# Performance work log

Measured on AMD Instinct MI355X. Metric: run time of the kernel, lower is better.

The kernel has to match this reference:

```python
import jax, jax.numpy as jnp
import numpy as np

ROPE_BASE = 1000000.0
EPS = 1e-6
N_HEADS = 8


def apply_rope(x, base=ROPE_BASE):
    # x: [b, s, h, d]
    b, s, h, d = x.shape
    half = d // 2
    theta = 1.0 / base ** (2 * jnp.arange(half) / d)          # [half]
    angles = jnp.arange(s)[:, None] * theta[None, :]          # [s, half]
    cos = jnp.cos(angles)[None, :, None, :]                   # [1, s, 1, half]
    sin = jnp.sin(angles)[None, :, None, :]
    x1, x2 = jnp.split(x, 2, axis=-1)
    return jnp.concatenate([x1 * cos - x2 * sin, x1 * sin + x2 * cos], axis=-1)


def setup_inputs() -> dict:
    key = jax.random.key(0)
    ks = jax.random.split(key, 5)
    b, s, dim = 2, 4096, 512
    x = jax.random.normal(ks[0], (b, s, dim), dtype=jnp.float32)
    scale = jnp.ones((dim,), dtype=jnp.float32)
    init = 1.0 / np.sqrt(dim)
    Wq = jax.random.normal(ks[1], (dim, dim), dtype=jnp.float32) * init
    Wk = jax.random.normal(ks[2], (dim, dim), dtype=jnp.float32) * init
    Wv = jax.random.normal(ks[3], (dim, dim), dtype=jnp.float32) * init
    Wo = jax.random.normal(ks[4], (dim, dim), dtype=jnp.float32) * init
    return {"x": x, "scale": scale, "Wq": Wq, "Wk": Wk, "Wv": Wv, "Wo": Wo}


def reference(x, scale, Wq, Wk, Wv, Wo):
    b, s, dim = x.shape
    h = N_HEADS
    dh = dim // h
    # RMSNorm (use_fast_variance=False path)
    variance = jnp.mean(x ** 2, axis=-1, keepdims=True)
    x_norm = x / jnp.sqrt(variance + EPS) * scale
    # Projections (flax Linear: y = x @ kernel, kernel [in, out])
    q = (x_norm @ Wq).reshape(b, s, h, dh)
    k = (x_norm @ Wk).reshape(b, s, h, dh)
    v = (x_norm @ Wv).reshape(b, s, h, dh)
    q = apply_rope(q)
    k = apply_rope(k)
    scores = jnp.einsum('bthd,bshd->bhts', q, k) / jnp.sqrt(jnp.float32(dh))
    mask = jnp.triu(jnp.full((s, s), -jnp.inf, dtype=jnp.float32), k=1)
    scores = scores + mask[None, None, :, :]
    attn = jax.nn.softmax(scores, axis=-1)
    out = jnp.einsum('bhts,bshd->bthd', attn, v).reshape(b, s, dim)
    return out @ Wo
```

## Files before the change

### kernel.cpp

```cpp
#include <hip/hip_runtime.h>
#include <hip/hip_bf16.h>

typedef _Float16 f16;
typedef _Float16 f16x2 __attribute__((ext_vector_type(2)));
typedef _Float16 f16x4 __attribute__((ext_vector_type(4)));
typedef _Float16 f16x8 __attribute__((ext_vector_type(8)));
typedef float f32x4 __attribute__((ext_vector_type(4)));

#define S_LEN 4096
#define DIM   512
#define NH    8
#define DH    64
#define BATCH 2
#define BHDIM (BATCH*NH)

#define QSCALE 0.18033688011112042f

__device__ __forceinline__ void gld16(const f16* g, f16* l) {
#if __has_builtin(__builtin_amdgcn_global_load_lds)
  __builtin_amdgcn_global_load_lds((const __attribute__((address_space(1))) void*)g,
                                   (__attribute__((address_space(3))) void*)l, 16, 0, 0);
#else
  *(f16x8*)l = *(const f16x8*)g;
#endif
}

__device__ __forceinline__ float fexp2(float x) {
#if __has_builtin(__builtin_amdgcn_exp2f)
  return __builtin_amdgcn_exp2f(x);
#else
  return exp2f(x);
#endif
}

__device__ __forceinline__ f16x2 pk2(float a, float b) {
#if __has_builtin(__builtin_amdgcn_cvt_pkrtz)
  auto r = __builtin_amdgcn_cvt_pkrtz(a, b);
  f16x2 o; __builtin_memcpy(&o, &r, sizeof(o));
  return o;
#else
  f16x2 r; r[0] = (f16)a; r[1] = (f16)b; return r;
#endif
}

__global__ __launch_bounds__(256) void rmsnorm_kernel(
    const float* __restrict__ x, const float* __restrict__ scale,
    f16* __restrict__ xn) {
  int row = blockIdx.x;
  int tid = threadIdx.x;
  const float* xr = x + (size_t)row * DIM;
  float2 v = *(const float2*)(xr + tid*2);
  float ss = v.x*v.x + v.y*v.y;
  #pragma unroll
  for (int off = 32; off > 0; off >>= 1) ss += __shfl_down(ss, off);
  __shared__ float red[4];
  if ((tid & 63) == 0) red[tid >> 6] = ss;
  __syncthreads();
  float tot = red[0] + red[1] + red[2] + red[3];
  float inv = rsqrtf(tot * (1.0f/DIM) + 1e-6f);
  float2 s = *(const float2*)(scale + tid*2);
  xn[(size_t)row*DIM + tid*2+0] = (f16)(v.x*inv*s.x);
  xn[(size_t)row*DIM + tid*2+1] = (f16)(v.y*inv*s.y);
}

__global__ void transpose_kernel(const float* __restrict__ Wq,
                                 const float* __restrict__ Wk,
                                 const float* __restrict__ Wv,
                                 const float* __restrict__ Wo,
                                 f16* __restrict__ wt_qkv, f16* __restrict__ wo_t) {
  __shared__ f16 tile[32][33];
  int mat = blockIdx.z;
  const float* src = (mat == 0) ? Wq : (mat == 1) ? Wk : (mat == 2) ? Wv : Wo;
  f16* dst = (mat < 3) ? (wt_qkv + (size_t)mat*DIM*DIM) : wo_t;
  int k0 = blockIdx.y * 32, n0 = blockIdx.x * 32;
  int tx = threadIdx.x, ty = threadIdx.y;
  #pragma unroll
  for (int i = 0; i < 32; i += 8)
    tile[ty+i][tx] = (f16)src[(size_t)(k0+ty+i)*DIM + n0+tx];
  __syncthreads();
  #pragma unroll
  for (int i = 0; i < 32; i += 8)
    dst[(size_t)(n0+ty+i)*DIM + k0+tx] = tile[tx][ty+i];
}

__global__ __launch_bounds__(256) void rope_table_kernel(float* __restrict__ ctab,
                                                         float* __restrict__ stab) {
  int idx = blockIdx.x*256 + threadIdx.x;
  int t = idx >> 5, d = idx & 31;
  float theta = exp2f(-(float)d * (19.931568569324174f / 32.0f));
  float sv, cv;
  sincosf((float)t * theta, &sv, &cv);
  ctab[idx] = cv; stab[idx] = sv;
}

__device__ __forceinline__ void gemm128_acc(
    const f16* __restrict__ A, const f16* __restrict__ Bt,
    int m0, int n0, f16* As, f16* Bs, f32x4 (&acc)[4][4]) {
  const int tid = threadIdx.x;
  const int wave = tid >> 6, lane = tid & 63;
  const int l16 = lane & 15, quad = lane >> 4;
  const int mrow = (wave & 1) * 64, ncol = (wave >> 1) * 64;
  const int srow = tid >> 3;
  const int gc = (tid & 7) ^ ((tid >> 3) & 7);

  for (int k0 = 0; k0 < DIM; k0 += 64) {
    if (k0) __syncthreads();
    #pragma unroll
    for (int i = 0; i < 4; i++) {
      gld16(A  + (size_t)(m0 + i*32 + srow)*DIM + k0 + gc*8, As + i*2048 + tid*8);
      gld16(Bt + (size_t)(n0 + i*32 + srow)*DIM + k0 + gc*8, Bs + i*2048 + tid*8);
    }
    __syncthreads();
    #pragma unroll
    for (int kc = 0; kc < 2; kc++) {
      f16x8 a[4], b[4];
      #pragma unroll
      for (int mt = 0; mt < 4; mt++) {
        int row = mrow + mt*16 + l16;
        a[mt] = *(const f16x8*)(As + row*64 + (((quad + 4*kc) ^ (l16 & 7)) * 8));
      }
      #pragma unroll
      for (int nt = 0; nt < 4; nt++) {
        int row = ncol + nt*16 + l16;
        b[nt] = *(const f16x8*)(Bs + row*64 + (((quad + 4*kc) ^ (l16 & 7)) * 8));
      }
      #pragma unroll
      for (int mt = 0; mt < 4; mt++)
        #pragma unroll
        for (int nt = 0; nt < 4; nt++)
          acc[mt][nt] = __builtin_amdgcn_mfma_f32_16x16x32_f16(a[mt], b[nt], acc[mt][nt], 0, 0, 0);
    }
  }
}

__global__ __launch_bounds__(256) void qkv_gemm_kernel(
    const f16* __restrict__ xn, const f16* __restrict__ wt,
    const float* __restrict__ ctab, const float* __restrict__ stab,
    f16* __restrict__ qbuf, f16* __restrict__ kbuf, f16* __restrict__ vt) {
  __shared__ __align__(16) f16 As[128*64], Bs[128*64];
  int m0 = blockIdx.x * 128, n0 = blockIdx.y * 128;
  f32x4 acc[4][4] = {};
  gemm128_acc(xn, wt, m0, n0, As, Bs, acc);

  const int tid = threadIdx.x;
  const int wave = tid >> 6, lane = tid & 63;
  const int l16 = lane & 15, quad = lane >> 4;
  int ncol = n0 + (wave >> 1) * 64;
  int which = ncol >> 9;
  int head = (ncol >> 6) & 7;
  int mbase = m0 + (wave & 1) * 64;

  if (which <= 1) {
    #pragma unroll
    for (int mt = 0; mt < 4; mt++)
      #pragma unroll
      for (int nt = 0; nt < 2; nt++) {
        int d = nt*16 + l16;
        #pragma unroll
        for (int r = 0; r < 4; r++) {
          int t = (mbase + mt*16 + quad*4 + r) & 4095;
          float cv = ctab[t*32 + d], sv = stab[t*32 + d];
          float x1 = acc[mt][nt][r], x2 = acc[mt][nt+2][r];
          acc[mt][nt][r]   = x1*cv - x2*sv;
          acc[mt][nt+2][r] = x1*sv + x2*cv;
        }
      }
  }
  if (which < 2) {
    float osc = (which == 0) ? QSCALE : 1.0f;
    f16* dst = which ? kbuf : qbuf;
    #pragma unroll
    for (int mt = 0; mt < 4; mt++)
      #pragma unroll
      for (int nt = 0; nt < 4; nt++)
        #pragma unroll
        for (int r = 0; r < 4; r++) {
          int m = mbase + mt*16 + quad*4 + r;
          int b = m >> 12, t = m & 4095;
          dst[(((size_t)(b*NH + head))*S_LEN + t)*DH + nt*16 + l16] = (f16)(acc[mt][nt][r]*osc);
        }
  } else {
    #pragma unroll
    for (int mt = 0; mt < 4; mt++)
      #pragma unroll
      for (int nt = 0; nt < 4; nt++) {
        int m = mbase + mt*16 + quad*4;
        int b = m >> 12, t = m & 4095;
        int d = nt*16 + l16;
        f16x4 v4 = {(f16)acc[mt][nt][0], (f16)acc[mt][nt][1],
                    (f16)acc[mt][nt][2], (f16)acc[mt][nt][3]};
        *(f16x4*)(vt + ((size_t)((b*NH + head)*DH + d))*S_LEN + t) = v4;
      }
  }
}

__global__ __launch_bounds__(128, 2) void attn_kernel(
    const f16* __restrict__ qbuf, const f16* __restrict__ kbuf,
    const f16* __restrict__ vtb, f16* __restrict__ ao) {
  int bid = blockIdx.x;
  int bh  = bid & 15;
  int p   = bid >> 4;

  int tid = threadIdx.x;
  int wave = tid >> 6, lane = tid & 63;
  int l16 = lane & 15, quad = lane >> 4;

  const f16* Q = qbuf + (size_t)bh*S_LEN*DH;
  const f16* K = kbuf + (size_t)bh*S_LEN*DH;
  const f16* V = vtb  + (size_t)bh*DH*S_LEN;

  int bandv[2] = {127 - p, p};
  int tcnt[2]  = {((127 - p) >> 1) + 1, (p >> 1) + 1};
  int rbase[2] = {bandv[0]*32 + wave*16, bandv[1]*32 + wave*16};

  f16x8 qa[2][2];
  #pragma unroll
  for (int bi = 0; bi < 2; bi++) {
    const f16* qrow = Q + (size_t)(rbase[bi] + l16)*DH + quad*8;
    qa[bi][0] = *(const f16x8*)(qrow);
    qa[bi][1] = *(const f16x8*)(qrow + 32);
  }

  f32x4 o[2][4] = {};
  float m_i[2] = {-1e30f, -1e30f};
  float l_i[2] = {0.f, 0.f};

  __shared__ __align__(16) f16 kt[2*4096];
  __shared__ __align__(16) f16 vs[2*4096];

  const int gcs = (tid & 7) ^ ((tid >> 3) & 7);
  const int srow = tid >> 3;

  #define STAGE(buf, kv)                                                        \
    do {                                                                        \
      f16* ktb = kt + (buf)*4096;                                               \
      f16* vsb = vs + (buf)*4096;                                               \
      _Pragma("unroll")                                                         \
      for (int n = 0; n < 4; n++) {                                             \
        gld16(K + (size_t)((kv) + n*16 + srow)*DH + gcs*8, ktb + n*1024 + tid*8);\
        gld16(V + (size_t)(n*16 + srow)*S_LEN + (kv) + gcs*8, vsb + n*1024 + tid*8);\
      }                                                                         \
    } while (0)

  STAGE(0, 0);
  __syncthreads();

  int nth = tcnt[0];
  for (int it = 0; it < nth; ++it) {
    int kv0 = it * 64;
    int cur = it & 1;
    if (it + 1 < nth) STAGE(cur ^ 1, kv0 + 64);

    const f16* ktc = kt + cur*4096;
    const f16* vsc = vs + cur*4096;

    bool act1 = (it < tcnt[1]);
    bool dia0 = (it == tcnt[0] - 1), dia1 = (it == tcnt[1] - 1);
    int ntl0 = dia0 ? ((bandv[0] & 1) ? 4 : 2) : 4;
    int ntl1 = act1 ? (dia1 ? ((bandv[1] & 1) ? 4 : 2) : 4) : 0;

    f32x4 st[2][4];
    #pragma unroll
    for (int nt = 0; nt < 4; nt++) {
      bool n0 = (nt < ntl0), n1 = (nt < ntl1);
      if (n0 || n1) {
        int row = nt*16 + l16;
        f16x8 kf0 = *(const f16x8*)(ktc + row*64 + (((quad)     ^ (row & 7))*8));
        f16x8 kf1 = *(const f16x8*)(ktc + row*64 + (((quad + 4) ^ (row & 7))*8));
        if (n0) {
          f32x4 z = {};
          z = __builtin_amdgcn_mfma_f32_16x16x32_f16(kf0, qa[0][0], z, 0, 0, 0);
          st[0][nt] = __builtin_amdgcn_mfma_f32_16x16x32_f16(kf1, qa[0][1], z, 0, 0, 0);
        }
        if (n1) {
          f32x4 z = {};
          z = __builtin_amdgcn_mfma_f32_16x16x32_f16(kf0, qa[1][0], z, 0, 0, 0);
          st[1][nt] = __builtin_amdgcn_mfma_f32_16x16x32_f16(kf1, qa[1][1], z, 0, 0, 0);
        }
      }
    }

    f16x8 pa[2][2];
    #pragma unroll
    for (int bi = 0; bi < 2; bi++) {
      int ntl = bi ? ntl1 : ntl0;
      if (ntl == 0) continue;
      bool diag = bi ? dia1 : dia0;
      int qglob = rbase[bi] + l16;
      float rmx = -1e30f;
      #pragma unroll
      for (int nt = 0; nt < 4; nt++) {
        if (nt >= ntl) continue;
        if (diag) {
          int kb = kv0 + nt*16 + quad*4;
          #pragma unroll
          for (int r = 0; r < 4; r++) {
            float v = st[bi][nt][r];
            if (kb + r > qglob) v = -1e30f;
            st[bi][nt][r] = v;
            rmx = fmaxf(rmx, v);
          }
        } else {
          #pragma unroll
          for (int r = 0; r < 4; r++) rmx = fmaxf(rmx, st[bi][nt][r]);
        }
      }
      rmx = fmaxf(rmx, __shfl_xor(rmx, 16));
      rmx = fmaxf(rmx, __shfl_xor(rmx, 32));
      if (!__all(rmx <= m_i[bi] + 8.0f)) {
        float mnew = fmaxf(m_i[bi], rmx);
        float alpha = fexp2(m_i[bi] - mnew);
        m_i[bi] = mnew;
        float al[4];
        #pragma unroll
        for (int r = 0; r < 4; r++) al[r] = __shfl(alpha, quad*4 + r);
        #pragma unroll
        for (int dnt = 0; dnt < 4; dnt++)
          #pragma unroll
          for (int r = 0; r < 4; r++) o[bi][dnt][r] *= al[r];
        l_i[bi] *= alpha;
      }
      float mref = m_i[bi];
      int kcl = ntl >> 1;
      float rs = 0.f;
      #pragma unroll
      for (int c = 0; c < 2; c++) {
        if (c >= kcl) continue;
        float e0 = fexp2(st[bi][2*c  ][0] - mref);
        float e1 = fexp2(st[bi][2*c  ][1] - mref);
        float e2 = fexp2(st[bi][2*c  ][2] - mref);
        float e3 = fexp2(st[bi][2*c  ][3] - mref);
        float e4 = fexp2(st[bi][2*c+1][0] - mref);
        float e5 = fexp2(st[bi][2*c+1][1] - mref);
        float e6 = fexp2(st[bi][2*c+1][2] - mref);
        float e7 = fexp2(st[bi][2*c+1][3] - mref);
        rs += ((e0+e1)+(e2+e3)) + ((e4+e5)+(e6+e7));
        f16x4 h0 = __builtin_shufflevector(pk2(e0,e1), pk2(e2,e3), 0,1,2,3);
        f16x4 h1 = __builtin_shufflevector(pk2(e4,e5), pk2(e6,e7), 0,1,2,3);
        pa[bi][c] = __builtin_shufflevector(h0, h1, 0,1,2,3,4,5,6,7);
      }
      l_i[bi] += rs;
    }

    int kcl0 = ntl0 >> 1, kcl1 = ntl1 >> 1;
    #pragma unroll
    for (int c = 0; c < 2; c++) {
      bool lv0 = (c < kcl0), lv1 = (c < kcl1);
      if (!lv0 && !lv1) continue;
      #pragma unroll
      for (int dnt = 0; dnt < 4; dnt++) {
        int vr = dnt*16 + l16;
        int iLo = vr*64 + (((c*4 +     (quad>>1)) ^ (vr & 7))*8) + (quad & 1)*4;
        int iHi = vr*64 + (((c*4 + 2 + (quad>>1)) ^ (vr & 7))*8) + (quad & 1)*4;
        f16x4 lo = *(const f16x4*)(vsc + iLo);
        f16x4 hi = *(const f16x4*)(vsc + iHi);
        f16x8 vf = __builtin_shufflevector(lo, hi, 0,1,2,3,4,5,6,7);
        if (lv0) o[0][dnt] = __builtin_amdgcn_mfma_f32_16x16x32_f16(pa[0][c], vf, o[0][dnt], 0, 0, 0);
        if (lv1) o[1][dnt] = __builtin_amdgcn_mfma_f32_16x16x32_f16(pa[1][c], vf, o[1][dnt], 0, 0, 0);
      }
    }

    __syncthreads();
  }
  #undef STAGE

  int b = bh >> 3, h = bh & 7;
  #pragma unroll
  for (int bi = 0; bi < 2; bi++) {
    float lf = l_i[bi];
    lf += __shfl_xor(lf, 16);
    lf += __shfl_xor(lf, 32);
    float lr[4];
    #pragma unroll
    for (int r = 0; r < 4; r++) lr[r] = __shfl(lf, quad*4 + r);
    #pragma unroll
    for (int r = 0; r < 4; r++) {
      float invl = 1.0f / lr[r];
      int t = rbase[bi] + quad*4 + r;
      size_t rowoff = ((size_t)(b*S_LEN + t))*DIM + h*DH;
      #pragma unroll
      for (int dnt = 0; dnt < 4; dnt++)
        ao[rowoff + dnt*16 + l16] = (f16)(o[bi][dnt][r]*invl);
    }
  }
}

__global__ __launch_bounds__(256) void out_gemm_kernel(
    const f16* __restrict__ ao, const f16* __restrict__ wot,
    float* __restrict__ out) {
  __shared__ __align__(16) f16 As[128*64], Bs[128*64];
  int m0 = blockIdx.x * 128, n0 = blockIdx.y * 128;
  f32x4 acc[4][4] = {};
  gemm128_acc(ao, wot, m0, n0, As, Bs, acc);

  const int tid = threadIdx.x;
  const int wave = tid >> 6, lane = tid & 63;
  const int l16 = lane & 15, quad = lane >> 4;
  int ncol = n0 + (wave >> 1) * 64;
  int mbase = m0 + (wave & 1) * 64;
  #pragma unroll
  for (int mt = 0; mt < 4; mt++)
    #pragma unroll
    for (int nt = 0; nt < 4; nt++)
      #pragma unroll
      for (int r = 0; r < 4; r++)
        out[(size_t)(mbase + mt*16 + quad*4 + r)*DIM + ncol + nt*16 + l16] = acc[mt][nt][r];
}

extern "C" void kernel_launch(void* const* d_in, const int* in_sizes, int n_in,
                              void* d_out, int out_size, void* d_ws, size_t ws_size,
                              hipStream_t stream) {
  const float* x     = (const float*)d_in[0];
  const float* scale = (const float*)d_in[1];
  const float* Wq    = (const float*)d_in[2];
  const float* Wk    = (const float*)d_in[3];
  const float* Wv    = (const float*)d_in[4];
  const float* Wo    = (const float*)d_in[5];
  float* out = (float*)d_out;

  const size_t ROWS = (size_t)BATCH * S_LEN;
  char* ws = (char*)d_ws;
  f16* xn     = (f16*)ws;  ws += ROWS * DIM * sizeof(f16);
  f16* wt_qkv = (f16*)ws;  ws += (size_t)3 * DIM * DIM * sizeof(f16);
  f16* wo_t   = (f16*)ws;  ws += (size_t)DIM * DIM * sizeof(f16);
  f16* qb     = (f16*)ws;  ws += (size_t)BHDIM * S_LEN * DH * sizeof(f16);
  f16* kb     = (f16*)ws;  ws += (size_t)BHDIM * S_LEN * DH * sizeof(f16);
  f16* vt     = (f16*)ws;  ws += (size_t)BHDIM * S_LEN * DH * sizeof(f16);
  float* ctab = (float*)ws; ws += (size_t)S_LEN * 32 * sizeof(float);
  float* stab = (float*)ws; ws += (size_t)S_LEN * 32 * sizeof(float);
  f16* ao     = xn;

  size_t need = (size_t)(ws - (char*)d_ws);
  if (ws_size < need) return;

  rmsnorm_kernel   <<<ROWS, 256, 0, stream>>>(x, scale, xn);
  transpose_kernel <<<dim3(16,16,4), dim3(32,8), 0, stream>>>(Wq, Wk, Wv, Wo, wt_qkv, wo_t);
  rope_table_kernel<<<512, 256, 0, stream>>>(ctab, stab);
  qkv_gemm_kernel  <<<dim3(64,12), 256, 0, stream>>>(xn, wt_qkv, ctab, stab, qb, kb, vt);
  attn_kernel      <<<1024, 128, 0, stream>>>(qb, kb, vt, ao);
  out_gemm_kernel  <<<dim3(64,4), 256, 0, stream>>>(ao, wo_t, out);
}
```

Measured before the change: 205.5 us.

## Split attention KV range across two blocks and merge partials in new kernel

Doubles the attention grid: each block now handles either the even or the odd 64-key tiles for its query bands, and writes partial outputs plus row max and row sum. A new merge kernel combines the two halves with log-sum-exp weights before the output GEMM. V is now stored in a pre-permuted layout so each lane loads its V fragments straight from global memory, which drops the V LDS staging. The row-max shuffles are also deferred to the rescale branch. This aims to raise occupancy and parallelism, at the cost of an extra kernel launch, f16 partial round-trips through memory, and uncached global V loads.

```diff
diff --git a/kernel.cpp b/kernel.cpp
--- a/kernel.cpp
+++ b/kernel.cpp
@@ -13,6 +13,7 @@
 #define DH    64
 #define BATCH 2
 #define BHDIM (BATCH*NH)
+#define ROWS2 (BHDIM*S_LEN)
 
 #define QSCALE 0.18033688011112042f
 
@@ -185,21 +186,26 @@
       #pragma unroll
       for (int nt = 0; nt < 4; nt++) {
         int m = mbase + mt*16 + quad*4;
-        int b = m >> 12, t = m & 4095;
+        int b = m >> 12, tcol = m & 4095;
+        int grp = tcol & ~63;
+        int pos = ((mt >> 1)*4 + quad)*8 + (mt & 1)*4;
         int d = nt*16 + l16;
         f16x4 v4 = {(f16)acc[mt][nt][0], (f16)acc[mt][nt][1],
                     (f16)acc[mt][nt][2], (f16)acc[mt][nt][3]};
-        *(f16x4*)(vt + ((size_t)((b*NH + head)*DH + d))*S_LEN + t) = v4;
+        *(f16x4*)(vt + ((size_t)((b*NH + head)*DH + d))*S_LEN + grp + pos) = v4;
       }
   }
 }
 
 __global__ __launch_bounds__(128, 2) void attn_kernel(
     const f16* __restrict__ qbuf, const f16* __restrict__ kbuf,
-    const f16* __restrict__ vtb, f16* __restrict__ ao) {
+    const f16* __restrict__ vtb, f16* __restrict__ po,
+    float* __restrict__ pm, float* __restrict__ pl) {
   int bid = blockIdx.x;
   int bh  = bid & 15;
-  int p   = bid >> 4;
+  int pp  = bid >> 4;
+  int p   = pp >> 1;
+  int hf  = pp & 1;
 
   int tid = threadIdx.x;
   int wave = tid >> 6, lane = tid & 63;
@@ -210,8 +216,10 @@
   const f16* V = vtb  + (size_t)bh*DH*S_LEN;
 
   int bandv[2] = {127 - p, p};
-  int tcnt[2]  = {((127 - p) >> 1) + 1, (p >> 1) + 1};
+  int T0 = ((127 - p) >> 1) + 1, T1 = (p >> 1) + 1;
   int rbase[2] = {bandv[0]*32 + wave*16, bandv[1]*32 + wave*16};
+
+  int nloc = (T0 - hf + 1) >> 1;
 
   f16x8 qa[2][2];
   #pragma unroll
@@ -226,36 +234,37 @@
   float l_i[2] = {0.f, 0.f};
 
   __shared__ __align__(16) f16 kt[2*4096];
-  __shared__ __align__(16) f16 vs[2*4096];
 
   const int gcs = (tid & 7) ^ ((tid >> 3) & 7);
   const int srow = tid >> 3;
 
-  #define STAGE(buf, kv)                                                        \
+  #define STAGEK(buf, kv)                                                       \
     do {                                                                        \
       f16* ktb = kt + (buf)*4096;                                               \
-      f16* vsb = vs + (buf)*4096;                                               \
       _Pragma("unroll")                                                         \
-      for (int n = 0; n < 4; n++) {                                             \
+      for (int n = 0; n < 4; n++)                                               \
         gld16(K + (size_t)((kv) + n*16 + srow)*DH + gcs*8, ktb + n*1024 + tid*8);\
-        gld16(V + (size_t)(n*16 + srow)*S_LEN + (kv) + gcs*8, vsb + n*1024 + tid*8);\
-      }                                                                         \
     } while (0)
 
-  STAGE(0, 0);
+  STAGEK(0, hf*64);
   __syncthreads();
 
-  int nth = tcnt[0];
-  for (int it = 0; it < nth; ++it) {
-    int kv0 = it * 64;
-    int cur = it & 1;
-    if (it + 1 < nth) STAGE(cur ^ 1, kv0 + 64);
+  for (int itl = 0; itl < nloc; ++itl) {
+    int g = 2*itl + hf;
+    int kv0 = g*64;
+    int cur = itl & 1;
+    if (itl + 1 < nloc) STAGEK(cur ^ 1, kv0 + 128);
+
+    f16x8 pv[2][4];
+    #pragma unroll
+    for (int c = 0; c < 2; c++)
+      #pragma unroll
+      for (int dnt = 0; dnt < 4; dnt++)
+        pv[c][dnt] = *(const f16x8*)(V + (size_t)(dnt*16 + l16)*S_LEN + kv0 + (c*4 + quad)*8);
 
     const f16* ktc = kt + cur*4096;
-    const f16* vsc = vs + cur*4096;
-
-    bool act1 = (it < tcnt[1]);
-    bool dia0 = (it == tcnt[0] - 1), dia1 = (it == tcnt[1] - 1);
+    bool act1 = (g < T1);
+    bool dia0 = (g == T0 - 1), dia1 = (g == T1 - 1);
     int ntl0 = dia0 ? ((bandv[0] & 1) ? 4 : 2) : 4;
     int ntl1 = act1 ? (dia1 ? ((bandv[1] & 1) ? 4 : 2) : 4) : 0;
 
@@ -305,10 +314,10 @@
           for (int r = 0; r < 4; r++) rmx = fmaxf(rmx, st[bi][nt][r]);
         }
       }
-      rmx = fmaxf(rmx, __shfl_xor(rmx, 16));
-      rmx = fmaxf(rmx, __shfl_xor(rmx, 32));
       if (!__all(rmx <= m_i[bi] + 8.0f)) {
-        float mnew = fmaxf(m_i[bi], rmx);
+        float rfull = fmaxf(rmx, __shfl_xor(rmx, 16));
+        rfull = fmaxf(rfull, __shfl_xor(rfull, 32));
+        float mnew = fmaxf(m_i[bi], rfull);
         float alpha = fexp2(m_i[bi] - mnew);
         m_i[bi] = mnew;
         float al[4];
@@ -349,40 +358,68 @@
       if (!lv0 && !lv1) continue;
       #pragma unroll
       for (int dnt = 0; dnt < 4; dnt++) {
-        int vr = dnt*16 + l16;
-        int iLo = vr*64 + (((c*4 +     (quad>>1)) ^ (vr & 7))*8) + (quad & 1)*4;
-        int iHi = vr*64 + (((c*4 + 2 + (quad>>1)) ^ (vr & 7))*8) + (quad & 1)*4;
-        f16x4 lo = *(const f16x4*)(vsc + iLo);
-        f16x4 hi = *(const f16x4*)(vsc + iHi);
-        f16x8 vf = __builtin_shufflevector(lo, hi, 0,1,2,3,4,5,6,7);
-        if (lv0) o[0][dnt] = __builtin_amdgcn_mfma_f32_16x16x32_f16(pa[0][c], vf, o[0][dnt], 0, 0, 0);
-        if (lv1) o[1][dnt] = __builtin_amdgcn_mfma_f32_16x16x32_f16(pa[1][c], vf, o[1][dnt], 0, 0, 0);
+        if (lv0) o[0][dnt] = __builtin_amdgcn_mfma_f32_16x16x32_f16(pa[0][c], pv[c][dnt], o[0][dnt], 0, 0, 0);
+        if (lv1) o[1][dnt] = __builtin_amdgcn_mfma_f32_16x16x32_f16(pa[1][c], pv[c][dnt], o[1][dnt], 0, 0, 0);
       }
     }
 
     __syncthreads();
   }
-  #undef STAGE
-
-  int b = bh >> 3, h = bh & 7;
+  #undef STAGEK
+
   #pragma unroll
   for (int bi = 0; bi < 2; bi++) {
     float lf = l_i[bi];
     lf += __shfl_xor(lf, 16);
     lf += __shfl_xor(lf, 32);
-    float lr[4];
+    if (quad == 0) {
+      int t = rbase[bi] + l16;
+      pm[(size_t)(hf*BHDIM + bh)*S_LEN + t] = m_i[bi];
+      pl[(size_t)(hf*BHDIM + bh)*S_LEN + t] = lf;
+    }
+    float lr[4], mrow[4];
     #pragma unroll
     for (int r = 0; r < 4; r++) lr[r] = __shfl(lf, quad*4 + r);
     #pragma unroll
     for (int r = 0; r < 4; r++) {
-      float invl = 1.0f / lr[r];
+      float invl = (lr[r] > 0.f) ? 1.0f / lr[r] : 0.f;
       int t = rbase[bi] + quad*4 + r;
-      size_t rowoff = ((size_t)(b*S_LEN + t))*DIM + h*DH;
+      size_t rowoff = ((size_t)(hf*BHDIM + bh)*S_LEN + t)*DH;
       #pragma unroll
       for (int dnt = 0; dnt < 4; dnt++)
-        ao[rowoff + dnt*16 + l16] = (f16)(o[bi][dnt][r]*invl);
-    }
-  }
+        po[rowoff + dnt*16 + l16] = (f16)(o[bi][dnt][r]*invl);
+    }
+    (void)mrow;
+  }
+}
+
+__global__ __launch_bounds__(256) void merge_kernel(
+    const f16* __restrict__ po, const float* __restrict__ pm,
+    const float* __restrict__ pl, f16* __restrict__ ao) {
+  int idx = blockIdx.x*256 + threadIdx.x;
+  int r_ = idx >> 2, q = idx & 3;
+  int bh = r_ >> 12, t = r_ & 4095;
+  float m0 = pm[r_], m1 = pm[ROWS2 + r_];
+  float l0 = pl[r_], l1 = pl[ROWS2 + r_];
+  float M  = fmaxf(m0, m1);
+  float a0 = l0 * fexp2(m0 - M);
+  float a1 = l1 * fexp2(m1 - M);
+  float inv = 1.0f / (a0 + a1);
+  float w0 = a0 * inv, w1 = a1 * inv;
+  const f16* p0 = po + (size_t)r_*DH + q*16;
+  const f16* p1 = po + (size_t)(ROWS2 + r_)*DH + q*16;
+  int b = bh >> 3, h = bh & 7;
+  f16* dst = ao + ((size_t)(b*S_LEN + t))*DIM + h*DH + q*16;
+  f16x8 v0a = *(const f16x8*)(p0), v0b = *(const f16x8*)(p0 + 8);
+  f16x8 v1a = *(const f16x8*)(p1), v1b = *(const f16x8*)(p1 + 8);
+  f16x8 oa, ob;
+  #pragma unroll
+  for (int j = 0; j < 8; j++) {
+    oa[j] = (f16)(w0*(float)v0a[j] + w1*(float)v1a[j]);
+    ob[j] = (f16)(w0*(float)v0b[j] + w1*(float)v1b[j]);
+  }
+  *(f16x8*)dst = oa;
+  *(f16x8*)(dst + 8) = ob;
 }
 
 __global__ __launch_bounds__(256) void out_gemm_kernel(
@@ -428,6 +465,9 @@
   f16* vt     = (f16*)ws;  ws += (size_t)BHDIM * S_LEN * DH * sizeof(f16);
   float* ctab = (float*)ws; ws += (size_t)S_LEN * 32 * sizeof(float);
   float* stab = (float*)ws; ws += (size_t)S_LEN * 32 * sizeof(float);
+  f16* po     = (f16*)ws;  ws += (size_t)2 * ROWS2 * DH * sizeof(f16);
+  float* pm   = (float*)ws; ws += (size_t)2 * ROWS2 * sizeof(float);
+  float* pl   = (float*)ws; ws += (size_t)2 * ROWS2 * sizeof(float);
   f16* ao     = xn;
 
   size_t need = (size_t)(ws - (char*)d_ws);
@@ -437,6 +477,7 @@
   transpose_kernel <<<dim3(16,16,4), dim3(32,8), 0, stream>>>(Wq, Wk, Wv, Wo, wt_qkv, wo_t);
   rope_table_kernel<<<512, 256, 0, stream>>>(ctab, stab);
   qkv_gemm_kernel  <<<dim3(64,12), 256, 0, stream>>>(xn, wt_qkv, ctab, stab, qb, kb, vt);
-  attn_kernel      <<<1024, 128, 0, stream>>>(qb, kb, vt, ao);
+  attn_kernel      <<<2048, 128, 0, stream>>>(qb, kb, vt, po, pm, pl);
+  merge_kernel     <<<1024, 256, 0, stream>>>(po, pm, pl, ao);
   out_gemm_kernel  <<<dim3(64,4), 256, 0, stream>>>(ao, wo_t, out);
 }
```

New measurement: 254.9 us. 24.0% more time.

## Merge prep kernels into one launch and permute V layout for single LDS loads

Applied to the files above, without the earlier changes.

Combines the RMSNorm, weight transpose/convert, and RoPE table kernels into one prep kernel dispatched by block index, removing two launches and their inter-kernel gaps. It also permutes the time order within each 64-token group of the transposed V buffer, so the attention kernel can fetch each MFMA B-operand with one 16-byte LDS read instead of two 8-byte reads plus a shuffle. The permutation has to line up exactly with the P-fragment ordering. If it does not, the results are wrong.

```diff
diff --git a/kernel.cpp b/kernel.cpp
--- a/kernel.cpp
+++ b/kernel.cpp
@@ -43,54 +43,52 @@
 #endif
 }
 
-__global__ __launch_bounds__(256) void rmsnorm_kernel(
+__global__ __launch_bounds__(256) void prep_kernel(
     const float* __restrict__ x, const float* __restrict__ scale,
-    f16* __restrict__ xn) {
-  int row = blockIdx.x;
+    const float* __restrict__ Wq, const float* __restrict__ Wk,
+    const float* __restrict__ Wv, const float* __restrict__ Wo,
+    f16* __restrict__ xn, f16* __restrict__ wt_qkv, f16* __restrict__ wo_t,
+    float* __restrict__ ctab, float* __restrict__ stab) {
+  int bid = blockIdx.x;
   int tid = threadIdx.x;
-  const float* xr = x + (size_t)row * DIM;
-  float2 v = *(const float2*)(xr + tid*2);
-  float ss = v.x*v.x + v.y*v.y;
-  #pragma unroll
-  for (int off = 32; off > 0; off >>= 1) ss += __shfl_down(ss, off);
-  __shared__ float red[4];
-  if ((tid & 63) == 0) red[tid >> 6] = ss;
-  __syncthreads();
-  float tot = red[0] + red[1] + red[2] + red[3];
-  float inv = rsqrtf(tot * (1.0f/DIM) + 1e-6f);
-  float2 s = *(const float2*)(scale + tid*2);
-  xn[(size_t)row*DIM + tid*2+0] = (f16)(v.x*inv*s.x);
-  xn[(size_t)row*DIM + tid*2+1] = (f16)(v.y*inv*s.y);
-}
-
-__global__ void transpose_kernel(const float* __restrict__ Wq,
-                                 const float* __restrict__ Wk,
-                                 const float* __restrict__ Wv,
-                                 const float* __restrict__ Wo,
-                                 f16* __restrict__ wt_qkv, f16* __restrict__ wo_t) {
-  __shared__ f16 tile[32][33];
-  int mat = blockIdx.z;
-  const float* src = (mat == 0) ? Wq : (mat == 1) ? Wk : (mat == 2) ? Wv : Wo;
-  f16* dst = (mat < 3) ? (wt_qkv + (size_t)mat*DIM*DIM) : wo_t;
-  int k0 = blockIdx.y * 32, n0 = blockIdx.x * 32;
-  int tx = threadIdx.x, ty = threadIdx.y;
-  #pragma unroll
-  for (int i = 0; i < 32; i += 8)
-    tile[ty+i][tx] = (f16)src[(size_t)(k0+ty+i)*DIM + n0+tx];
-  __syncthreads();
-  #pragma unroll
-  for (int i = 0; i < 32; i += 8)
-    dst[(size_t)(n0+ty+i)*DIM + k0+tx] = tile[tx][ty+i];
-}
-
-__global__ __launch_bounds__(256) void rope_table_kernel(float* __restrict__ ctab,
-                                                         float* __restrict__ stab) {
-  int idx = blockIdx.x*256 + threadIdx.x;
-  int t = idx >> 5, d = idx & 31;
-  float theta = exp2f(-(float)d * (19.931568569324174f / 32.0f));
-  float sv, cv;
-  sincosf((float)t * theta, &sv, &cv);
-  ctab[idx] = cv; stab[idx] = sv;
+  if (bid < 8192) {
+    const float* xr = x + (size_t)bid * DIM;
+    float2 v = *(const float2*)(xr + tid*2);
+    float ss = v.x*v.x + v.y*v.y;
+    #pragma unroll
+    for (int off = 32; off > 0; off >>= 1) ss += __shfl_down(ss, off);
+    __shared__ float red[4];
+    if ((tid & 63) == 0) red[tid >> 6] = ss;
+    __syncthreads();
+    float tot = red[0] + red[1] + red[2] + red[3];
+    float inv = rsqrtf(tot * (1.0f/DIM) + 1e-6f);
+    float2 s = *(const float2*)(scale + tid*2);
+    xn[(size_t)bid*DIM + tid*2+0] = (f16)(v.x*inv*s.x);
+    xn[(size_t)bid*DIM + tid*2+1] = (f16)(v.y*inv*s.y);
+  } else if (bid < 9216) {
+    __shared__ f16 tile[32][33];
+    int b2 = bid - 8192;
+    int mat = b2 >> 8;
+    int rem = b2 & 255;
+    int k0 = (rem >> 4) * 32, n0 = (rem & 15) * 32;
+    const float* src = (mat == 0) ? Wq : (mat == 1) ? Wk : (mat == 2) ? Wv : Wo;
+    f16* dst = (mat < 3) ? (wt_qkv + (size_t)mat*DIM*DIM) : wo_t;
+    int tx = tid & 31, ty = tid >> 5;
+    #pragma unroll
+    for (int i = 0; i < 32; i += 8)
+      tile[ty+i][tx] = (f16)src[(size_t)(k0+ty+i)*DIM + n0+tx];
+    __syncthreads();
+    #pragma unroll
+    for (int i = 0; i < 32; i += 8)
+      dst[(size_t)(n0+ty+i)*DIM + k0+tx] = tile[tx][ty+i];
+  } else {
+    int idx = (bid - 9216)*256 + tid;
+    int t = idx >> 5, d = idx & 31;
+    float theta = exp2f(-(float)d * (19.931568569324174f / 32.0f));
+    float sv, cv;
+    sincosf((float)t * theta, &sv, &cv);
+    ctab[idx] = cv; stab[idx] = sv;
+  }
 }
 
 __device__ __forceinline__ void gemm128_acc(
@@ -185,11 +183,13 @@
       #pragma unroll
       for (int nt = 0; nt < 4; nt++) {
         int m = mbase + mt*16 + quad*4;
-        int b = m >> 12, t = m & 4095;
+        int b = m >> 12, tcol = m & 4095;
+        int grp = tcol & ~63;
+        int pos = ((mt >> 1)*4 + quad)*8 + (mt & 1)*4;
         int d = nt*16 + l16;
         f16x4 v4 = {(f16)acc[mt][nt][0], (f16)acc[mt][nt][1],
                     (f16)acc[mt][nt][2], (f16)acc[mt][nt][3]};
-        *(f16x4*)(vt + ((size_t)((b*NH + head)*DH + d))*S_LEN + t) = v4;
+        *(f16x4*)(vt + ((size_t)((b*NH + head)*DH + d))*S_LEN + grp + pos) = v4;
       }
   }
 }
@@ -350,11 +350,7 @@
       #pragma unroll
       for (int dnt = 0; dnt < 4; dnt++) {
         int vr = dnt*16 + l16;
-        int iLo = vr*64 + (((c*4 +     (quad>>1)) ^ (vr & 7))*8) + (quad & 1)*4;
-        int iHi = vr*64 + (((c*4 + 2 + (quad>>1)) ^ (vr & 7))*8) + (quad & 1)*4;
-        f16x4 lo = *(const f16x4*)(vsc + iLo);
-        f16x4 hi = *(const f16x4*)(vsc + iHi);
-        f16x8 vf = __builtin_shufflevector(lo, hi, 0,1,2,3,4,5,6,7);
+        f16x8 vf = *(const f16x8*)(vsc + vr*64 + (((c*4 + quad) ^ (vr & 7))*8));
         if (lv0) o[0][dnt] = __builtin_amdgcn_mfma_f32_16x16x32_f16(pa[0][c], vf, o[0][dnt], 0, 0, 0);
         if (lv1) o[1][dnt] = __builtin_amdgcn_mfma_f32_16x16x32_f16(pa[1][c], vf, o[1][dnt], 0, 0, 0);
       }
@@ -433,10 +429,9 @@
   size_t need = (size_t)(ws - (char*)d_ws);
   if (ws_size < need) return;
 
-  rmsnorm_kernel   <<<ROWS, 256, 0, stream>>>(x, scale, xn);
-  transpose_kernel <<<dim3(16,16,4), dim3(32,8), 0, stream>>>(Wq, Wk, Wv, Wo, wt_qkv, wo_t);
-  rope_table_kernel<<<512, 256, 0, stream>>>(ctab, stab);
-  qkv_gemm_kernel  <<<dim3(64,12), 256, 0, stream>>>(xn, wt_qkv, ctab, stab, qb, kb, vt);
-  attn_kernel      <<<1024, 128, 0, stream>>>(qb, kb, vt, ao);
-  out_gemm_kernel  <<<dim3(64,4), 256, 0, stream>>>(ao, wo_t, out);
-}
+  prep_kernel    <<<9728, 256, 0, stream>>>(x, scale, Wq, Wk, Wv, Wo,
+                                            xn, wt_qkv, wo_t, ctab, stab);
+  qkv_gemm_kernel<<<dim3(64,12), 256, 0, stream>>>(xn, wt_qkv, ctab, stab, qb, kb, vt);
+  attn_kernel    <<<1024, 128, 0, stream>>>(qb, kb, vt, ao);
+  out_gemm_kernel<<<dim3(64,4), 256, 0, stream>>>(ao, wo_t, out);
+}
```

New measurement: 200.5 us. 2.4% less time.
